# Optimization experiments

Hardware: AMD Instinct MI355X
Metric: run time of the kernel (lower is better)

## Reference

```python
import jax, jax.numpy as jnp
from jax import lax
import numpy as np

D_MODEL = 512
D_INNER = 1024
DT_RANK = 32
D_STATE = 16
D_CONV = 3
B, L = 2, 1024
SQ = 4  # sqrt(d_state)


def setup_inputs() -> dict:
    key = jax.random.key(0)
    ks = jax.random.split(key, 16)
    s = lambda *sh: 1.0 / np.sqrt(sh[-1])
    inp = {
        "x": jax.random.normal(ks[0], (B, L, D_MODEL), jnp.float32),
        "h": jax.random.normal(ks[1], (B, L, D_INNER, D_STATE), jnp.float32),
        "in_proj_w": jax.random.normal(ks[2], (2 * D_INNER, D_MODEL), jnp.float32) * s(D_MODEL),
        "conv1d_w": jax.random.normal(ks[3], (D_INNER, 1, D_CONV), jnp.float32) * 0.3,
        "conv1d_b": jax.random.normal(ks[4], (D_INNER,), jnp.float32) * 0.02,
        "x_proj_w": jax.random.normal(ks[5], (DT_RANK + 2 * D_STATE, D_INNER), jnp.float32) * s(D_INNER),
        "dt_proj_w": jax.random.normal(ks[6], (D_INNER, DT_RANK), jnp.float32) * s(DT_RANK),
        "dt_proj_b": jax.random.normal(ks[7], (D_INNER,), jnp.float32) * 0.1 - 4.0,
        "A_log": jnp.log(jnp.tile(jnp.arange(1, D_STATE + 1, dtype=jnp.float32), (D_INNER, 1))),
        "D": jnp.ones((D_INNER,), jnp.float32),
        "sf1_w": jax.random.normal(ks[8], (D_INNER, 1, 1, 1), jnp.float32) * 0.3,
        "sf1_b": jax.random.normal(ks[9], (D_INNER,), jnp.float32) * 0.02,
        "sf2_w": jax.random.normal(ks[10], (D_INNER, 1, 3, 3), jnp.float32) * 0.3,
        "sf2_b": jax.random.normal(ks[11], (D_INNER,), jnp.float32) * 0.02,
        "alpha": jnp.ones((2,), jnp.float32),
        "out_proj_w": jax.random.normal(ks[12], (D_MODEL, D_INNER), jnp.float32) * s(D_INNER),
    }
    return inp


def _dwconv1d(x_bdl, w, b):
    # x: [B, D, L], w: [D, 1, K], groups=D, SAME padding (K=3, pad=1)
    y = lax.conv_general_dilated(x_bdl, w, (1,), [(1, 1)],
                                 dimension_numbers=("NCH", "OIH", "NCH"),
                                 feature_group_count=D_INNER)
    return y + b[None, :, None]


def _dwconv2d(x, w, b, pad):
    y = lax.conv_general_dilated(x, w, (1, 1), [(pad, pad), (pad, pad)],
                                 dimension_numbers=("NCHW", "OIHW", "NCHW"),
                                 feature_group_count=D_INNER)
    return y + b[None, :, None, None]


def reference(x, h, in_proj_w, conv1d_w, conv1d_b, x_proj_w, dt_proj_w, dt_proj_b,
              A_log, D, sf1_w, sf1_b, sf2_w, sf2_b, alpha, out_proj_w):
    # in_proj -> split x/z
    xz = x @ in_proj_w.T                       # [B, L, 2*Di]
    xc, z = jnp.split(xz, 2, axis=-1)
    # depthwise causal-ish conv1d over L
    xc = _dwconv1d(jnp.transpose(xc, (0, 2, 1)), conv1d_w, conv1d_b)
    xs = jax.nn.silu(jnp.transpose(xc, (0, 2, 1)))  # [B, L, Di]

    # ssm_step
    A = -jnp.exp(A_log)                         # [Di, S]
    dBC = xs @ x_proj_w.T                       # [B, L, R+2S]
    delta, Bm, Cm = jnp.split(dBC, [DT_RANK, DT_RANK + D_STATE], axis=-1)
    delta = jax.nn.softplus(delta @ dt_proj_w.T + dt_proj_b)  # [B, L, Di]
    deltaA = jnp.exp(delta[..., None] * A)      # [B, L, Di, S]
    BX = (delta * xs)[..., None] * Bm[:, :, None, :]
    hn = deltaA * h + BX                        # [B, L, Di, S]

    # state fusion: reshape state dim S into 4x4 spatial, depthwise 1x1 + 3x3 convs
    h2 = hn.reshape(B * L, D_INNER, SQ, SQ)
    hf = alpha[0] * _dwconv2d(h2, sf1_w, sf1_b, 0) + alpha[1] * _dwconv2d(h2, sf2_w, sf2_b, 1)
    hn = hf.reshape(B, L, D_INNER, D_STATE)

    y = jnp.einsum("blds,bls->bld", hn, Cm) + D * xs
    out = (y * jax.nn.silu(z)) @ out_proj_w.T   # [B, L, Dm]
    return out, hn
```

## Files before the change

kernel.cpp:

```cpp
#include <hip/hip_runtime.h>
#include <stdint.h>

#define BLT 2048
#define DMODEL 512
#define DINNER 1024
#define TCH 2

typedef __bf16 bf16x8 __attribute__((ext_vector_type(8)));
typedef float f32x4 __attribute__((ext_vector_type(4)));

__global__ __launch_bounds__(256) void gemm_mfma_64(const float* __restrict__ A,
                                                    const float* __restrict__ B,
                                                    float* __restrict__ C,
                                                    int M, int N, int K) {
    __shared__ __bf16 As[64][72];
    __shared__ __bf16 Bs[64][72];
    const int tid = threadIdx.x;
    const int wave = tid >> 6, lane = tid & 63;
    const int waveM = wave >> 1, waveN = wave & 1;
    const int quad = lane >> 4, l16 = lane & 15;

    const int nwg = gridDim.x * gridDim.y;
    const int bid = blockIdx.y * gridDim.x + blockIdx.x;
    const int cpx = nwg >> 3;
    const int swz = (bid & 7) * cpx + (bid >> 3);
    const int bx = swz % gridDim.x, by = swz / gridDim.x;
    const int m0 = by * 64, n0 = bx * 64;

    f32x4 acc[2][2];
#pragma unroll
    for (int mi = 0; mi < 2; mi++)
#pragma unroll
        for (int ni = 0; ni < 2; ni++) acc[mi][ni] = (f32x4){0.f, 0.f, 0.f, 0.f};

    const int sr = tid >> 4;
    const int sc = (tid & 15) * 4;

    for (int k0 = 0; k0 < K; k0 += 64) {
#pragma unroll
        for (int p = 0; p < 4; p++) {
            int r = sr + p * 16;
            float4 v = *(const float4*)(A + (size_t)(m0 + r) * K + k0 + sc);
            union { __bf16 b[4]; uint2 u; } pk;
            pk.b[0] = (__bf16)v.x; pk.b[1] = (__bf16)v.y;
            pk.b[2] = (__bf16)v.z; pk.b[3] = (__bf16)v.w;
            *(uint2*)&As[r][sc] = pk.u;
        }
#pragma unroll
        for (int p = 0; p < 4; p++) {
            int r = sr + p * 16;
            float4 v = *(const float4*)(B + (size_t)(n0 + r) * K + k0 + sc);
            union { __bf16 b[4]; uint2 u; } pk;
            pk.b[0] = (__bf16)v.x; pk.b[1] = (__bf16)v.y;
            pk.b[2] = (__bf16)v.z; pk.b[3] = (__bf16)v.w;
            *(uint2*)&Bs[r][sc] = pk.u;
        }
        __syncthreads();
#pragma unroll
        for (int kk = 0; kk < 64; kk += 32) {
            bf16x8 af[2], bfr[2];
#pragma unroll
            for (int mi = 0; mi < 2; mi++)
                af[mi] = *(const bf16x8*)&As[waveM * 32 + mi * 16 + l16][kk + quad * 8];
#pragma unroll
            for (int ni = 0; ni < 2; ni++)
                bfr[ni] = *(const bf16x8*)&Bs[waveN * 32 + ni * 16 + l16][kk + quad * 8];
#pragma unroll
            for (int mi = 0; mi < 2; mi++)
#pragma unroll
                for (int ni = 0; ni < 2; ni++)
                    acc[mi][ni] = __builtin_amdgcn_mfma_f32_16x16x32_bf16(
                        af[mi], bfr[ni], acc[mi][ni], 0, 0, 0);
        }
        __syncthreads();
    }
#pragma unroll
    for (int mi = 0; mi < 2; mi++)
#pragma unroll
        for (int ni = 0; ni < 2; ni++)
#pragma unroll
            for (int reg = 0; reg < 4; reg++) {
                int m = m0 + waveM * 32 + mi * 16 + quad * 4 + reg;
                int n = n0 + waveN * 32 + ni * 16 + l16;
                C[(size_t)m * N + n] = acc[mi][ni][reg];
            }
}

__global__ __launch_bounds__(256) void gemm_mfma_s_splitk(const float* __restrict__ A,
                                                          const float* __restrict__ B,
                                                          float* __restrict__ Cpart,
                                                          int M, int N, int K, int kchunk) {
    __shared__ __bf16 As[32][72];
    __shared__ __bf16 Bs[64][72];
    const int tid = threadIdx.x;
    const int wave = tid >> 6, lane = tid & 63;
    const int waveM = wave >> 1, waveN = wave & 1;
    const int quad = lane >> 4, l16 = lane & 15;
    const int m0 = blockIdx.y * 32, n0 = blockIdx.x * 64;
    const int kbeg = blockIdx.z * kchunk;
    const int kend = kbeg + kchunk;

    f32x4 acc[2];
    acc[0] = (f32x4){0.f, 0.f, 0.f, 0.f};
    acc[1] = (f32x4){0.f, 0.f, 0.f, 0.f};

    const int sr = tid >> 4;
    const int sc = (tid & 15) * 4;

    for (int k0 = kbeg; k0 < kend; k0 += 64) {
#pragma unroll
        for (int p = 0; p < 2; p++) {
            int r = sr + p * 16;
            float4 v = *(const float4*)(A + (size_t)(m0 + r) * K + k0 + sc);
            union { __bf16 b[4]; uint2 u; } pk;
            pk.b[0] = (__bf16)v.x; pk.b[1] = (__bf16)v.y;
            pk.b[2] = (__bf16)v.z; pk.b[3] = (__bf16)v.w;
            *(uint2*)&As[r][sc] = pk.u;
        }
#pragma unroll
        for (int p = 0; p < 4; p++) {
            int r = sr + p * 16;
            float4 v = *(const float4*)(B + (size_t)(n0 + r) * K + k0 + sc);
            union { __bf16 b[4]; uint2 u; } pk;
            pk.b[0] = (__bf16)v.x; pk.b[1] = (__bf16)v.y;
            pk.b[2] = (__bf16)v.z; pk.b[3] = (__bf16)v.w;
            *(uint2*)&Bs[r][sc] = pk.u;
        }
        __syncthreads();
#pragma unroll
        for (int kk = 0; kk < 64; kk += 32) {
            bf16x8 af = *(const bf16x8*)&As[waveM * 16 + l16][kk + quad * 8];
#pragma unroll
            for (int ni = 0; ni < 2; ni++) {
                bf16x8 bf = *(const bf16x8*)&Bs[waveN * 32 + ni * 16 + l16][kk + quad * 8];
                acc[ni] = __builtin_amdgcn_mfma_f32_16x16x32_bf16(af, bf, acc[ni], 0, 0, 0);
            }
        }
        __syncthreads();
    }
    float* Cz = Cpart + (size_t)blockIdx.z * M * N;
#pragma unroll
    for (int ni = 0; ni < 2; ni++)
#pragma unroll
        for (int reg = 0; reg < 4; reg++) {
            int m = m0 + waveM * 16 + quad * 4 + reg;
            int n = n0 + waveN * 32 + ni * 16 + l16;
            Cz[(size_t)m * N + n] = acc[ni][reg];
        }
}

__global__ __launch_bounds__(256) void prep_k(const float* __restrict__ dtw,
                                              const float* __restrict__ A_log,
                                              float* __restrict__ dtwT,
                                              float* __restrict__ Aneg) {
    int i = blockIdx.x * 256 + threadIdx.x;
    {
        int r = i >> 10, d = i & 1023;
        dtwT[i] = dtw[d * 32 + r];
    }
    if (i < 16384) Aneg[i] = -__expf(A_log[i]);
}

__global__ __launch_bounds__(256) void conv1d_silu_k(const float* __restrict__ xz,
                                                     const float* __restrict__ w,
                                                     const float* __restrict__ bias,
                                                     float* __restrict__ xs) {
    int idx = blockIdx.x * 256 + threadIdx.x;
    int t = idx >> 10, d = idx & 1023;
    int l = t & 1023;
    float cur = xz[(size_t)t * 2048 + d];
    float prev = (l > 0) ? xz[(size_t)(t - 1) * 2048 + d] : 0.f;
    float nxt = (l < 1023) ? xz[(size_t)(t + 1) * 2048 + d] : 0.f;
    float v = w[d * 3] * prev + w[d * 3 + 1] * cur + w[d * 3 + 2] * nxt + bias[d];
    xs[idx] = v / (1.f + __expf(-v));
}

__global__ __launch_bounds__(256) void ssm_fuse_k(
    const float* __restrict__ h,
    const float* __restrict__ xz,
    const float* __restrict__ xs,
    const float* __restrict__ dBCp,
    const float* __restrict__ dtwT,
    const float* __restrict__ dtb,
    const float* __restrict__ Aneg,
    const float* __restrict__ Dp,
    const float* __restrict__ sf1w, const float* __restrict__ sf1b,
    const float* __restrict__ sf2w, const float* __restrict__ sf2b,
    const float* __restrict__ alpha,
    float* __restrict__ hn_out,
    float* __restrict__ yz) {
    const int tid = threadIdx.x;
    const int d = blockIdx.x * 256 + tid;
    const int t0 = blockIdx.y * TCH;

    __shared__ float dbc_s[TCH * 64];
    if (tid < TCH * 64) {
        const size_t o = (size_t)t0 * 64 + tid;
        const size_t st = (size_t)BLT * 64;
        dbc_s[tid] = dBCp[o] + dBCp[o + st] + dBCp[o + 2 * st] + dBCp[o + 3 * st];
    }
    __syncthreads();

    float dtw_r[32];
#pragma unroll
    for (int r = 0; r < 32; r++) dtw_r[r] = dtwT[r * 1024 + d];
    float an[16];
    {
        const float4* apv = (const float4*)(Aneg + (size_t)d * 16);
#pragma unroll
        for (int q = 0; q < 4; q++) {
            float4 aq = apv[q];
            an[q * 4 + 0] = aq.x; an[q * 4 + 1] = aq.y;
            an[q * 4 + 2] = aq.z; an[q * 4 + 3] = aq.w;
        }
    }
    float w2[9];
#pragma unroll
    for (int k = 0; k < 9; k++) w2[k] = sf2w[d * 9 + k];
    const float w1 = sf1w[d], b1 = sf1b[d], b2v = sf2b[d];
    const float a0f = alpha[0], a1f = alpha[1];
    const float dtb_d = dtb[d], Dp_d = Dp[d];

#pragma unroll
    for (int tt = 0; tt < TCH; tt++) {
        const int t = t0 + tt;
        const size_t td = (size_t)t * 1024 + d;
        const float xv = xs[td];
        const float zv = xz[(size_t)t * 2048 + 1024 + d];
        float hv[16];
        {
            const float4* hp = (const float4*)(h + td * 16);
#pragma unroll
            for (int q = 0; q < 4; q++) {
                float4 hq = hp[q];
                hv[q * 4 + 0] = hq.x; hv[q * 4 + 1] = hq.y;
                hv[q * 4 + 2] = hq.z; hv[q * 4 + 3] = hq.w;
            }
        }
        float accd = dtb_d;
#pragma unroll
        for (int r = 0; r < 32; r++) accd += dbc_s[tt * 64 + r] * dtw_r[r];
        const float dt = (accd > 20.f) ? accd : __logf(1.f + __expf(accd));
        const float dx = dt * xv;

        float hn[16];
#pragma unroll
        for (int s = 0; s < 16; s++)
            hn[s] = __expf(dt * an[s]) * hv[s] + dx * dbc_s[tt * 64 + 32 + s];

        float hf[16];
#pragma unroll
        for (int i = 0; i < 4; i++)
#pragma unroll
            for (int j = 0; j < 4; j++) {
                float s2 = b2v;
#pragma unroll
                for (int ki = 0; ki < 3; ki++)
#pragma unroll
                    for (int kj = 0; kj < 3; kj++) {
                        int ii = i + ki - 1, jj = j + kj - 1;
                        if (ii >= 0 && ii < 4 && jj >= 0 && jj < 4)
                            s2 += hn[ii * 4 + jj] * w2[ki * 3 + kj];
                    }
                hf[i * 4 + j] = a0f * (w1 * hn[i * 4 + j] + b1) + a1f * s2;
            }
        float y = Dp_d * xv;
#pragma unroll
        for (int s = 0; s < 16; s++) y += hf[s] * dbc_s[tt * 64 + 48 + s];
        yz[td] = y * (zv / (1.f + __expf(-zv)));
        float4* op = (float4*)(hn_out + td * 16);
#pragma unroll
        for (int q = 0; q < 4; q++)
            op[q] = make_float4(hf[q * 4 + 0], hf[q * 4 + 1], hf[q * 4 + 2], hf[q * 4 + 3]);
    }
}

extern "C" void kernel_launch(void* const* d_in, const int* in_sizes, int n_in,
                              void* d_out, int out_size, void* d_ws, size_t ws_size,
                              hipStream_t stream) {
    const float* x         = (const float*)d_in[0];
    const float* h         = (const float*)d_in[1];
    const float* in_proj_w = (const float*)d_in[2];
    const float* conv1d_w  = (const float*)d_in[3];
    const float* conv1d_b  = (const float*)d_in[4];
    const float* x_proj_w  = (const float*)d_in[5];
    const float* dt_proj_w = (const float*)d_in[6];
    const float* dt_proj_b = (const float*)d_in[7];
    const float* A_log     = (const float*)d_in[8];
    const float* Dp        = (const float*)d_in[9];
    const float* sf1w      = (const float*)d_in[10];
    const float* sf1b      = (const float*)d_in[11];
    const float* sf2w      = (const float*)d_in[12];
    const float* sf2b      = (const float*)d_in[13];
    const float* alpha     = (const float*)d_in[14];
    const float* out_projw = (const float*)d_in[15];

    float* out0   = (float*)d_out;
    float* hn_out = out0 + (size_t)BLT * DMODEL;

    float* xz   = (float*)d_ws;
    float* xs   = xz + (size_t)BLT * 2048;
    float* dBCp = xs + (size_t)BLT * DINNER;
    float* yz   = dBCp + (size_t)4 * BLT * 64;
    float* dtwT = yz + (size_t)BLT * DINNER;
    float* Aneg = dtwT + 32 * 1024;

    prep_k<<<128, 256, 0, stream>>>(dt_proj_w, A_log, dtwT, Aneg);
    gemm_mfma_64<<<dim3(2048 / 64, BLT / 64), 256, 0, stream>>>(x, in_proj_w, xz,
                                                                BLT, 2048, DMODEL);
    conv1d_silu_k<<<(BLT * DINNER) / 256, 256, 0, stream>>>(xz, conv1d_w, conv1d_b, xs);
    gemm_mfma_s_splitk<<<dim3(1, BLT / 32, 4), 256, 0, stream>>>(xs, x_proj_w, dBCp,
                                                                 BLT, 64, DINNER, 256);
    ssm_fuse_k<<<dim3(4, BLT / TCH), 256, 0, stream>>>(h, xz, xs, dBCp, dtwT, dt_proj_b,
                                                       Aneg, Dp, sf1w, sf1b, sf2w, sf2b, alpha,
                                                       hn_out, yz);
    gemm_mfma_64<<<dim3(DMODEL / 64, BLT / 64), 256, 0, stream>>>(yz, out_projw, out0,
                                                                  BLT, DMODEL, DINNER);
}
```

Before: 397.0 us.

## Stage dt_proj weights in LDS, vectorize conv1d, and double SSM time chunk

The SSM fusion kernel now loads the dt_proj weight tile into padded shared memory with coalesced float4 reads instead of keeping 32 registers per thread. That removes the separate transpose step from the prep kernel. The time chunk per block doubles, so all 256 threads fill dbc_s, and the kernel gets a launch_bounds occupancy hint. The conv1d+SiLU kernel is vectorized to four channels per thread. Trade-offs: more LDS traffic in the inner dot product and fewer blocks in the SSM grid.

```diff
diff --git a/kernel.cpp b/kernel.cpp
--- a/kernel.cpp
+++ b/kernel.cpp
@@ -4,7 +4,7 @@
 #define BLT 2048
 #define DMODEL 512
 #define DINNER 1024
-#define TCH 2
+#define TCH 4
 
 typedef __bf16 bf16x8 __attribute__((ext_vector_type(8)));
 typedef float f32x4 __attribute__((ext_vector_type(4)));
@@ -149,15 +149,9 @@
         }
 }
 
-__global__ __launch_bounds__(256) void prep_k(const float* __restrict__ dtw,
-                                              const float* __restrict__ A_log,
-                                              float* __restrict__ dtwT,
+__global__ __launch_bounds__(256) void prep_k(const float* __restrict__ A_log,
                                               float* __restrict__ Aneg) {
     int i = blockIdx.x * 256 + threadIdx.x;
-    {
-        int r = i >> 10, d = i & 1023;
-        dtwT[i] = dtw[d * 32 + r];
-    }
     if (i < 16384) Aneg[i] = -__expf(A_log[i]);
 }
 
@@ -166,21 +160,37 @@
                                                      const float* __restrict__ bias,
                                                      float* __restrict__ xs) {
     int idx = blockIdx.x * 256 + threadIdx.x;
-    int t = idx >> 10, d = idx & 1023;
+    int t = idx >> 8, d0 = (idx & 255) * 4;
     int l = t & 1023;
-    float cur = xz[(size_t)t * 2048 + d];
-    float prev = (l > 0) ? xz[(size_t)(t - 1) * 2048 + d] : 0.f;
-    float nxt = (l < 1023) ? xz[(size_t)(t + 1) * 2048 + d] : 0.f;
-    float v = w[d * 3] * prev + w[d * 3 + 1] * cur + w[d * 3 + 2] * nxt + bias[d];
-    xs[idx] = v / (1.f + __expf(-v));
-}
-
-__global__ __launch_bounds__(256) void ssm_fuse_k(
+    const float4 cur = *(const float4*)(xz + (size_t)t * 2048 + d0);
+    float4 prev = make_float4(0.f, 0.f, 0.f, 0.f);
+    float4 nxt = make_float4(0.f, 0.f, 0.f, 0.f);
+    if (l > 0)    prev = *(const float4*)(xz + (size_t)(t - 1) * 2048 + d0);
+    if (l < 1023) nxt  = *(const float4*)(xz + (size_t)(t + 1) * 2048 + d0);
+    const float4 bv = *(const float4*)(bias + d0);
+    const float4 wa = *(const float4*)(w + d0 * 3);
+    const float4 wb = *(const float4*)(w + d0 * 3 + 4);
+    const float4 wc = *(const float4*)(w + d0 * 3 + 8);
+    float pr[4] = {prev.x, prev.y, prev.z, prev.w};
+    float cu[4] = {cur.x, cur.y, cur.z, cur.w};
+    float nx[4] = {nxt.x, nxt.y, nxt.z, nxt.w};
+    float bb[4] = {bv.x, bv.y, bv.z, bv.w};
+    float wf[12] = {wa.x, wa.y, wa.z, wa.w, wb.x, wb.y, wb.z, wb.w, wc.x, wc.y, wc.z, wc.w};
+    float out[4];
+#pragma unroll
+    for (int j = 0; j < 4; j++) {
+        float v = wf[j * 3] * pr[j] + wf[j * 3 + 1] * cu[j] + wf[j * 3 + 2] * nx[j] + bb[j];
+        out[j] = v / (1.f + __expf(-v));
+    }
+    *(float4*)(xs + (size_t)t * 1024 + d0) = make_float4(out[0], out[1], out[2], out[3]);
+}
+
+__global__ __launch_bounds__(256, 4) void ssm_fuse_k(
     const float* __restrict__ h,
     const float* __restrict__ xz,
     const float* __restrict__ xs,
     const float* __restrict__ dBCp,
-    const float* __restrict__ dtwT,
+    const float* __restrict__ dtw,
     const float* __restrict__ dtb,
     const float* __restrict__ Aneg,
     const float* __restrict__ Dp,
@@ -190,20 +200,32 @@
     float* __restrict__ hn_out,
     float* __restrict__ yz) {
     const int tid = threadIdx.x;
-    const int d = blockIdx.x * 256 + tid;
+    const int d0b = blockIdx.x * 256;
+    const int d = d0b + tid;
     const int t0 = blockIdx.y * TCH;
 
+    __shared__ float dtw_s[256][33];
     __shared__ float dbc_s[TCH * 64];
-    if (tid < TCH * 64) {
+
+    {
         const size_t o = (size_t)t0 * 64 + tid;
         const size_t st = (size_t)BLT * 64;
         dbc_s[tid] = dBCp[o] + dBCp[o + st] + dBCp[o + 2 * st] + dBCp[o + 3 * st];
     }
+    {
+        const float4* src = (const float4*)(dtw + (size_t)d0b * 32);
+#pragma unroll
+        for (int c = 0; c < 8; c++) {
+            int f4 = c * 256 + tid;
+            float4 v = src[f4];
+            int dl = f4 >> 3;
+            int r0 = (f4 & 7) << 2;
+            float* wp = &dtw_s[dl][r0];
+            wp[0] = v.x; wp[1] = v.y; wp[2] = v.z; wp[3] = v.w;
+        }
+    }
     __syncthreads();
 
-    float dtw_r[32];
-#pragma unroll
-    for (int r = 0; r < 32; r++) dtw_r[r] = dtwT[r * 1024 + d];
     float an[16];
     {
         const float4* apv = (const float4*)(Aneg + (size_t)d * 16);
@@ -239,7 +261,7 @@
         }
         float accd = dtb_d;
 #pragma unroll
-        for (int r = 0; r < 32; r++) accd += dbc_s[tt * 64 + r] * dtw_r[r];
+        for (int r = 0; r < 32; r++) accd += dbc_s[tt * 64 + r] * dtw_s[tid][r];
         const float dt = (accd > 20.f) ? accd : __logf(1.f + __expf(accd));
         const float dx = dt * xv;
 
@@ -302,16 +324,15 @@
     float* xs   = xz + (size_t)BLT * 2048;
     float* dBCp = xs + (size_t)BLT * DINNER;
     float* yz   = dBCp + (size_t)4 * BLT * 64;
-    float* dtwT = yz + (size_t)BLT * DINNER;
-    float* Aneg = dtwT + 32 * 1024;
-
-    prep_k<<<128, 256, 0, stream>>>(dt_proj_w, A_log, dtwT, Aneg);
+    float* Aneg = yz + (size_t)BLT * DINNER;
+
+    prep_k<<<64, 256, 0, stream>>>(A_log, Aneg);
     gemm_mfma_64<<<dim3(2048 / 64, BLT / 64), 256, 0, stream>>>(x, in_proj_w, xz,
                                                                 BLT, 2048, DMODEL);
-    conv1d_silu_k<<<(BLT * DINNER) / 256, 256, 0, stream>>>(xz, conv1d_w, conv1d_b, xs);
+    conv1d_silu_k<<<(BLT * DINNER / 4) / 256, 256, 0, stream>>>(xz, conv1d_w, conv1d_b, xs);
     gemm_mfma_s_splitk<<<dim3(1, BLT / 32, 4), 256, 0, stream>>>(xs, x_proj_w, dBCp,
                                                                  BLT, 64, DINNER, 256);
-    ssm_fuse_k<<<dim3(4, BLT / TCH), 256, 0, stream>>>(h, xz, xs, dBCp, dtwT, dt_proj_b,
+    ssm_fuse_k<<<dim3(4, BLT / TCH), 256, 0, stream>>>(h, xz, xs, dBCp, dt_proj_w, dt_proj_b,
                                                        Aneg, Dp, sf1w, sf1b, sf2w, sf2b, alpha,
                                                        hn_out, yz);
     gemm_mfma_64<<<dim3(DMODEL / 64, BLT / 64), 256, 0, stream>>>(yz, out_projw, out0,
```

After: 397.0 us. Within noise of the previous version (-0.0%).
